# Performance work log

Hardware: AMD Instinct MI355X
Metric: run time of the kernel (lower is better)

The kernel has to match this reference:

```python
import jax, jax.numpy as jnp
import numpy as np

BLANK = 0          # tf.nn.ctc_loss default blank_index (StringLookup reserves 0 for OOV)
PAD = 127          # padding_value = char_to_num.vocabulary_size()
NEG = -1e30        # log-space 'zero' (avoid -inf to keep grads NaN-free)
B, T, C, L = 1024, 256, 128, 32


def setup_inputs() -> dict:
    key = jax.random.key(0)
    k1, k2 = jax.random.split(key)
    # labels in [1, PAD-1]; none equal PAD so label_length == L (full-length labels)
    y_true = jax.random.randint(k1, (B, L), 1, PAD).astype(jnp.int32)
    y_pred = jax.random.normal(k2, (B, T, C), dtype=jnp.float32)
    return {"y_true": y_true, "y_pred": y_pred}


def _ctc_loss(y_true, y_pred):
    """Faithful jax version of tf.nn.ctc_loss(labels, logits, label_len, T,
    logits_time_major=False, blank_index=0): standard log-space alpha DP."""
    Bn, Tn, Cn = y_pred.shape
    Ln = y_true.shape[1]
    S = 2 * Ln + 1  # extended label length (blanks interleaved)

    logp = jax.nn.log_softmax(y_pred, axis=-1)                    # [B,T,C]

    # extended label sequence: blank, l1, blank, l2, ..., blank   # [B,S]
    ext = jnp.full((Bn, S), BLANK, dtype=y_true.dtype)
    ext = ext.at[:, 1::2].set(y_true)

    # log-probs gathered at extended-label symbols                # [B,T,S]
    lp_ext = jnp.take_along_axis(
        logp, jnp.broadcast_to(ext[:, None, :], (Bn, Tn, S)), axis=2)

    # label_length = count of non-padding entries (mirrors count_nonzero)
    label_len = jnp.sum(y_true != PAD, axis=1)                    # [B]

    # skip transition s-2 -> s allowed iff ext[s] is a non-blank differing
    # from ext[s-2]
    skip_ok = jnp.concatenate(
        [jnp.zeros((Bn, 2), bool),
         (ext[:, 2:] != BLANK) & (ext[:, 2:] != ext[:, :-2])], axis=1)  # [B,S]

    neg1 = jnp.full((Bn, 1), NEG, logp.dtype)
    neg2 = jnp.full((Bn, 2), NEG, logp.dtype)

    alpha0 = jnp.full((Bn, S), NEG, logp.dtype)
    alpha0 = alpha0.at[:, 0].set(lp_ext[:, 0, 0]).at[:, 1].set(lp_ext[:, 0, 1])

    def step(alpha, lp_t):  # alpha,[B,S]  lp_t,[B,S]
        a1 = jnp.concatenate([neg1, alpha[:, :-1]], axis=1)
        a2 = jnp.concatenate([neg2, alpha[:, :-2]], axis=1)
        a2 = jnp.where(skip_ok, a2, NEG)
        new = lp_t + jnp.logaddexp(jnp.logaddexp(alpha, a1), a2)
        return new, None

    lp_seq = jnp.transpose(lp_ext, (1, 0, 2))                     # [T,B,S]
    alphaT, _ = jax.lax.scan(step, alpha0, lp_seq[1:])            # [B,S]

    # total log-likelihood ends at last blank (2*len) or last label (2*len-1)
    bi = jnp.arange(Bn)
    e1 = 2 * label_len
    e2 = 2 * label_len - 1
    loglik = jnp.logaddexp(alphaT[bi, e1], alphaT[bi, e2])        # [B]
    return -loglik


def reference(y_true, y_pred):
    # The original layer returns y_pred and registers the loss via add_loss;
    # the compute-dominant quantity is the per-example CTC loss, returned here.
    return _ctc_loss(y_true, y_pred)
```

## Files before the change

### kernel.cpp

```cpp
#include <hip/hip_runtime.h>
#include <cstdint>


#define CTC_BLANK 0
#define CTC_PAD   127
#define NEG       (-1e30f)
#define LOG2E     1.44269504088896340736f
#define LN2       0.69314718055994530942f

constexpr int Bn = 1024, Tn = 256, Cn = 128, Ln = 32;
constexpr int NSLOT = Ln + 1;
constexpr int CR  = 16;
constexpr int NCH = Tn / CR;
constexpr int CF  = CR * Cn;

__device__ __forceinline__ float fexp2(float x) { return __builtin_amdgcn_exp2f(x); }
__device__ __forceinline__ float flog2(float x) { return __builtin_amdgcn_logf(x); }

template <int CTRL>
__device__ __forceinline__ float dpp_add(float s) {
    int v = __builtin_amdgcn_update_dpp(0, __float_as_int(s), CTRL, 0xF, 0xF, true);
    return s + __int_as_float(v);
}
__device__ __forceinline__ float dpp_wave_shr1(float src, float old) {
    return __int_as_float(__builtin_amdgcn_update_dpp(
        __float_as_int(old), __float_as_int(src), 0x138, 0xF, 0xF, false));
}
__device__ __forceinline__ void gl_lds16(const float* g, float* l) {
    __builtin_amdgcn_global_load_lds(
        (const __attribute__((address_space(1))) uint32_t*)g,
        (__attribute__((address_space(3))) uint32_t*)l, 16, 0, 0);
}

__global__ __launch_bounds__(512, 8) void ctc_fused_kernel(
        const int*   __restrict__ y_true,
        const float* __restrict__ y_pred,
        float*       __restrict__ out)
{
    __shared__ __align__(16) float raw[2][CF];
    __shared__ _Float16 Gc[Tn * NSLOT];
    __shared__ int   labels[Ln];
    __shared__ __align__(16) int cmap[Cn];
    __shared__ int   used[Cn];
    __shared__ int   wcnt[8];
    __shared__ float partS[16];

    const int b    = blockIdx.x;
    const int tid  = threadIdx.x;
    const int lane = tid & 63;
    const int wave = tid >> 6;

    const float* gbase = y_pred + (size_t)b * Tn * Cn;

    auto stage = [&](int c, int buf) {
        gl_lds16(gbase + c * CF + tid * 4, &raw[buf][wave * 256]);
    };

    stage(0, 0);

    if (tid < Ln) labels[tid] = y_true[b * Ln + tid];
    if (tid < Cn) used[tid] = 0;
    __syncthreads();
    if (tid == 0) used[CTC_BLANK] = 1;
    if (tid < Ln) used[labels[tid]] = 1;
    __syncthreads();
    {
        bool f = (tid < Cn) && (used[tid] != 0);
        unsigned long long m = __ballot(f);
        if (lane == 0) wcnt[wave] = __popcll(m);
        __syncthreads();
        int base = 0;
        for (int w = 0; w < wave; ++w) base += wcnt[w];
        if (tid < Cn)
            cmap[tid] = f ? (base + __popcll(m & ((1ull << lane) - 1ull))) : -1;
        __syncthreads();
    }

    const int half = lane >> 5;
    const int l32  = lane & 31;
    const int4 cm  = ((const int4*)cmap)[l32];
    float acc = 0.f;

    const int  i      = lane;
    const bool validO = (i < Ln);
    const bool validE = (i <= Ln);
    const int  myLab   = validO ? labels[i] : -1;
    const int  prevLab = (i >= 1 && i < Ln) ? labels[i - 1] : -1;
    const int  slotO   = validO ? cmap[myLab] : 0;
    const bool skipO   = (i >= 1 && i < Ln) &&
                         (myLab != CTC_BLANK) && (myLab != prevLab);
    const int  len = __popcll(__ballot(validO && (myLab != CTC_PAD)));
    float aE = NEG, aO = NEG;

    auto dp_chunk = [&](int t0, int t1) {
        int t = t0;
        if (t == 0) {
            aE = (i == 0) ? (float)Gc[0]     : NEG;
            aO = (i == 0) ? (float)Gc[slotO] : NEG;
            t = 1;
        }
        float pB[2], pO[2];
        const int ta = t, tb = (t + 1 < t1) ? t + 1 : t1 - 1;
        pB[0] = (float)Gc[ta * NSLOT]; pO[0] = (float)Gc[ta * NSLOT + slotO];
        pB[1] = (float)Gc[tb * NSLOT]; pO[1] = (float)Gc[tb * NSLOT + slotO];
        int k = 0;
        #pragma unroll 2
        for (; t < t1; ++t) {
            const float lpB = pB[k], lpO = pO[k];
            const int tp = (t + 2 < t1) ? t + 2 : t1 - 1;
            pB[k] = (float)Gc[tp * NSLOT];
            pO[k] = (float)Gc[tp * NSLOT + slotO];
            k ^= 1;

            const float aOup = dpp_wave_shr1(aO, NEG);
            const float m  = fmaxf(aE, aOup);
            const float e1 = fexp2(aE - m);
            const float e2 = fexp2(aOup - m);
            const float sE = e1 + e2;
            const float nE = lpB + m + flog2(sE);
            const float m3 = fmaxf(aO, m);
            const float nO = lpO + m3 +
                flog2(fexp2(aO - m3) + (skipO ? sE : e1) * fexp2(m - m3));
            aE = validE ? nE : NEG;
            aO = validO ? nO : NEG;
        }
    };

    for (int c = 0; c < NCH; ++c) {
        if (c + 1 < NCH) stage(c + 1, (c + 1) & 1);

        if (wave == 0 && c > 0) dp_chunk((c - 1) * CR, c * CR);

        __builtin_amdgcn_sched_barrier(0);
        if (c + 1 < NCH) asm volatile("s_waitcnt vmcnt(1)" ::: "memory");
        else             asm volatile("s_waitcnt vmcnt(0)" ::: "memory");
        __builtin_amdgcn_sched_barrier(0);

        {
            const int rl = 2 * wave + half;
            const int r  = c * CR + rl;
            const float4 x = ((const float4*)&raw[c & 1][rl * Cn])[l32];
            const float e0 = x.x * LOG2E, e1 = x.y * LOG2E,
                        e2 = x.z * LOG2E, e3 = x.w * LOG2E;
            if (cm.x >= 0) Gc[r * NSLOT + cm.x] = (_Float16)e0;
            if (cm.y >= 0) Gc[r * NSLOT + cm.y] = (_Float16)e1;
            if (cm.z >= 0) Gc[r * NSLOT + cm.z] = (_Float16)e2;
            if (cm.w >= 0) Gc[r * NSLOT + cm.w] = (_Float16)e3;
            float s = fexp2(e0) + fexp2(e1) + fexp2(e2) + fexp2(e3);
            s = dpp_add<0x111>(s);
            s = dpp_add<0x112>(s);
            s = dpp_add<0x114>(s);
            s = dpp_add<0x118>(s);
            s = dpp_add<0x142>(s);
            acc += flog2(s);
        }
        if (c == NCH - 1 && l32 == 31) partS[wave * 2 + half] = acc;

        asm volatile("s_waitcnt lgkmcnt(0)" ::: "memory");
        __builtin_amdgcn_s_barrier();
    }

    if (wave == 0) {
        dp_chunk(Tn - CR, Tn);
        const float v1 = __shfl(aE, len, 64);
        const float v2 = __shfl(aO, len - 1, 64);
        if (i == 0) {
            float S = 0.f;
            #pragma unroll
            for (int j = 0; j < 16; ++j) S += partS[j];
            const float mm = fmaxf(v1, v2);
            const float L2 = mm + flog2(fexp2(v1 - mm) + fexp2(v2 - mm));
            out[b] = LN2 * (S - L2);
        }
    }
}

extern "C" void kernel_launch(void* const* d_in, const int* in_sizes, int n_in,
                              void* d_out, int out_size, void* d_ws, size_t ws_size,
                              hipStream_t stream) {
    const int*   y_true = (const int*)d_in[0];
    const float* y_pred = (const float*)d_in[1];
    float*       out    = (float*)d_out;
    ctc_fused_kernel<<<Bn, 512, 0, stream>>>(y_true, y_pred, out);
}
```

Before: 202.1 us.

## Deepen per-wave prefetch to four stages and batch DP into four phases

Each wave now owns a private ring of four LDS staging slots and keeps several global-to-LDS loads in flight. This removes the block-wide barrier that previously sat between every 16-row chunk. The alpha DP in wave 0 now runs only at four phase boundaries over 64 timesteps each, so only four block barriers remain. The aim is more memory-level parallelism and less synchronisation, at the cost of more LDS per block (the occupancy hint drops from 8 to 6) and longer serial DP stretches while the other waves idle.

New measurement: 214.1 us. +5.9%, slower.

```diff
diff --git a/kernel.cpp b/kernel.cpp
--- a/kernel.cpp
+++ b/kernel.cpp
@@ -10,9 +10,12 @@
 
 constexpr int Bn = 1024, Tn = 256, Cn = 128, Ln = 32;
 constexpr int NSLOT = Ln + 1;
-constexpr int CR  = 16;
-constexpr int NCH = Tn / CR;
-constexpr int CF  = CR * Cn;
+constexpr int CR    = 16;
+constexpr int NIT   = Tn / CR;
+constexpr int DEPTH = 4;
+constexpr int PH    = 4;
+constexpr int IPP   = NIT / PH;
+constexpr int TPP   = Tn / PH;
 
 __device__ __forceinline__ float fexp2(float x) { return __builtin_amdgcn_exp2f(x); }
 __device__ __forceinline__ float flog2(float x) { return __builtin_amdgcn_logf(x); }
@@ -32,12 +35,12 @@
         (__attribute__((address_space(3))) uint32_t*)l, 16, 0, 0);
 }
 
-__global__ __launch_bounds__(512, 8) void ctc_fused_kernel(
+__global__ __launch_bounds__(512, 6) void ctc_fused_kernel(
         const int*   __restrict__ y_true,
         const float* __restrict__ y_pred,
         float*       __restrict__ out)
 {
-    __shared__ __align__(16) float raw[2][CF];
+    __shared__ __align__(16) float raw[8][DEPTH][256];
     __shared__ _Float16 Gc[Tn * NSLOT];
     __shared__ int   labels[Ln];
     __shared__ __align__(16) int cmap[Cn];
@@ -52,11 +55,13 @@
 
     const float* gbase = y_pred + (size_t)b * Tn * Cn;
 
-    auto stage = [&](int c, int buf) {
-        gl_lds16(gbase + c * CF + tid * 4, &raw[buf][wave * 256]);
+    auto stage = [&](int j) {
+        gl_lds16(gbase + (size_t)(j * CR + 2 * wave) * Cn + lane * 4,
+                 &raw[wave][j & (DEPTH - 1)][0]);
     };
 
-    stage(0, 0);
+    #pragma unroll
+    for (int j0 = 0; j0 < DEPTH; ++j0) stage(j0);
 
     if (tid < Ln) labels[tid] = y_true[b * Ln + tid];
     if (tid < Cn) used[tid] = 0;
@@ -126,20 +131,19 @@
         }
     };
 
-    for (int c = 0; c < NCH; ++c) {
-        if (c + 1 < NCH) stage(c + 1, (c + 1) & 1);
+    for (int p = 0; p < PH; ++p) {
+        for (int q = 0; q < IPP; ++q) {
+            const int j   = p * IPP + q;
+            const int rem = (NIT - 1) - j;
+            if (rem >= DEPTH - 1) asm volatile("s_waitcnt vmcnt(3)" ::: "memory");
+            else if (rem == 2)    asm volatile("s_waitcnt vmcnt(2)" ::: "memory");
+            else if (rem == 1)    asm volatile("s_waitcnt vmcnt(1)" ::: "memory");
+            else                  asm volatile("s_waitcnt vmcnt(0)" ::: "memory");
 
-        if (wave == 0 && c > 0) dp_chunk((c - 1) * CR, c * CR);
-
-        __builtin_amdgcn_sched_barrier(0);
-        if (c + 1 < NCH) asm volatile("s_waitcnt vmcnt(1)" ::: "memory");
-        else             asm volatile("s_waitcnt vmcnt(0)" ::: "memory");
-        __builtin_amdgcn_sched_barrier(0);
-
-        {
-            const int rl = 2 * wave + half;
-            const int r  = c * CR + rl;
-            const float4 x = ((const float4*)&raw[c & 1][rl * Cn])[l32];
+            const int slot = j & (DEPTH - 1);
+            const int r    = j * CR + 2 * wave + half;
+            const float4 x =
+                ((const float4*)&raw[wave][slot][0])[half * 32 + l32];
             const float e0 = x.x * LOG2E, e1 = x.y * LOG2E,
                         e2 = x.z * LOG2E, e3 = x.w * LOG2E;
             if (cm.x >= 0) Gc[r * NSLOT + cm.x] = (_Float16)e0;
@@ -153,15 +157,20 @@
             s = dpp_add<0x118>(s);
             s = dpp_add<0x142>(s);
             acc += flog2(s);
+            if (j == NIT - 1 && l32 == 31) partS[wave * 2 + half] = acc;
+
+            asm volatile("s_waitcnt lgkmcnt(0)" ::: "memory");
+            if (j + DEPTH < NIT) stage(j + DEPTH);
         }
-        if (c == NCH - 1 && l32 == 31) partS[wave * 2 + half] = acc;
+
+        if (wave == 0 && p > 0) dp_chunk((p - 1) * TPP, p * TPP);
 
         asm volatile("s_waitcnt lgkmcnt(0)" ::: "memory");
         __builtin_amdgcn_s_barrier();
     }
 
     if (wave == 0) {
-        dp_chunk(Tn - CR, Tn);
+        dp_chunk(Tn - TPP, Tn);
         const float v1 = __shfl(aE, len, 64);
         const float v2 = __shfl(aO, len - 1, 64);
         if (i == 0) {
```

## Split CTC into softmax kernel and packed 4-waves-per-block DP kernel via workspace

Applied to the files above, without the earlier changes.

Replaces the single fused kernel, in which one wave per block ran the serial alpha recursion while the others streamed logits, with two kernels. The first computes the log-sum-exp and writes the gathered log-probs as a slot-major fp16 table to the workspace. The second runs the DP with four batch items per 256-thread block and vectorised h4 loads. This is meant to stop the serial DP from holding a 512-thread block resident, and to let many more DP waves run concurrently. In exchange it adds a global round trip for the gathered table (about 17 MB), a second launch, and a dependence on the workspace size, with the old fused kernel kept as a fallback.

Result: slower. 227.3 us (+12.5%).

```diff
diff --git a/kernel.cpp b/kernel.cpp
--- a/kernel.cpp
+++ b/kernel.cpp
@@ -10,9 +10,13 @@
 
 constexpr int Bn = 1024, Tn = 256, Cn = 128, Ln = 32;
 constexpr int NSLOT = Ln + 1;
-constexpr int CR  = 16;
-constexpr int NCH = Tn / CR;
-constexpr int CF  = CR * Cn;
+constexpr int GSLOT = 34;
+constexpr int GT_B  = GSLOT * Tn;
+
+constexpr size_t WS_GT   = 0;
+constexpr size_t WS_SLOT = (size_t)Bn * GT_B * 2;
+constexpr size_t WS_S    = WS_SLOT + (size_t)Bn * Ln * 4;
+constexpr size_t WS_NEED = WS_S + (size_t)Bn * 4;
 
 __device__ __forceinline__ float fexp2(float x) { return __builtin_amdgcn_exp2f(x); }
 __device__ __forceinline__ float flog2(float x) { return __builtin_amdgcn_logf(x); }
@@ -32,7 +36,180 @@
         (__attribute__((address_space(3))) uint32_t*)l, 16, 0, 0);
 }
 
-__global__ __launch_bounds__(512, 8) void ctc_fused_kernel(
+__global__ __launch_bounds__(512, 8) void ctc_softmax_kernel(
+        const int*   __restrict__ y_true,
+        const float* __restrict__ y_pred,
+        _Float16*    __restrict__ Gt,
+        int*         __restrict__ slotO_arr,
+        float*       __restrict__ Sglob)
+{
+    __shared__ int labels[Ln];
+    __shared__ __align__(16) int cmap[Cn];
+    __shared__ int used[Cn];
+    __shared__ int wcnt[8];
+    __shared__ float partS[16];
+
+    const int b    = blockIdx.x;
+    const int tid  = threadIdx.x;
+    const int lane = tid & 63;
+    const int wave = tid >> 6;
+    const int half = lane >> 5;
+    const int l32  = lane & 31;
+
+    const float4* gsrc = (const float4*)(y_pred + (size_t)b * Tn * Cn);
+    float4 xr0 = gsrc[tid];
+    float4 xr1 = gsrc[512  + tid];
+    float4 xr2 = gsrc[1024 + tid];
+    float4 xr3 = gsrc[1536 + tid];
+
+    if (tid < Ln) labels[tid] = y_true[b * Ln + tid];
+    if (tid < Cn) used[tid] = 0;
+    __syncthreads();
+    if (tid == 0) used[CTC_BLANK] = 1;
+    if (tid < Ln) used[labels[tid]] = 1;
+    __syncthreads();
+    {
+        bool f = (tid < Cn) && (used[tid] != 0);
+        unsigned long long m = __ballot(f);
+        if (lane == 0) wcnt[wave] = __popcll(m);
+        __syncthreads();
+        int base = 0;
+        for (int w = 0; w < wave; ++w) base += wcnt[w];
+        if (tid < Cn)
+            cmap[tid] = f ? (base + __popcll(m & ((1ull << lane) - 1ull))) : -1;
+        __syncthreads();
+    }
+
+    const int4 cm = ((const int4*)cmap)[l32];
+    _Float16* gt = Gt + (size_t)b * GT_B;
+    const int rbase = tid >> 5;
+    float acc = 0.f;
+
+    #pragma unroll
+    for (int j = 0; j < 16; ++j) {
+        float4 x;
+        if      ((j & 3) == 0) x = xr0;
+        else if ((j & 3) == 1) x = xr1;
+        else if ((j & 3) == 2) x = xr2;
+        else                   x = xr3;
+        if (j + 4 < 16) {
+            float4 nx = gsrc[(j + 4) * 512 + tid];
+            if      ((j & 3) == 0) xr0 = nx;
+            else if ((j & 3) == 1) xr1 = nx;
+            else if ((j & 3) == 2) xr2 = nx;
+            else                   xr3 = nx;
+        }
+        const float e0 = x.x * LOG2E, e1 = x.y * LOG2E,
+                    e2 = x.z * LOG2E, e3 = x.w * LOG2E;
+        const int tcol = j * 16 + rbase;
+        if (cm.x >= 0) gt[cm.x * Tn + tcol] = (_Float16)e0;
+        if (cm.y >= 0) gt[cm.y * Tn + tcol] = (_Float16)e1;
+        if (cm.z >= 0) gt[cm.z * Tn + tcol] = (_Float16)e2;
+        if (cm.w >= 0) gt[cm.w * Tn + tcol] = (_Float16)e3;
+        float s = fexp2(e0) + fexp2(e1) + fexp2(e2) + fexp2(e3);
+        s = dpp_add<0x111>(s);
+        s = dpp_add<0x112>(s);
+        s = dpp_add<0x114>(s);
+        s = dpp_add<0x118>(s);
+        s = dpp_add<0x142>(s);
+        acc += flog2(s);
+    }
+    if (l32 == 31) partS[wave * 2 + half] = acc;
+    if (tid < Ln) slotO_arr[b * Ln + tid] = cmap[labels[tid]];
+    __syncthreads();
+    if (tid == 0) {
+        float S = 0.f;
+        #pragma unroll
+        for (int j = 0; j < 16; ++j) S += partS[j];
+        Sglob[b] = S;
+    }
+}
+
+typedef __attribute__((ext_vector_type(4))) _Float16 h4;
+
+__global__ __launch_bounds__(256) void ctc_dp_kernel(
+        const int*      __restrict__ y_true,
+        const _Float16* __restrict__ Gt,
+        const int*      __restrict__ slotO_arr,
+        const float*    __restrict__ Sglob,
+        float*          __restrict__ out)
+{
+    const int wave = threadIdx.x >> 6;
+    const int i    = threadIdx.x & 63;
+    const int b    = blockIdx.x * 4 + wave;
+    if (b >= Bn) return;
+
+    const bool validO = (i < Ln);
+    const bool validE = (i <= Ln);
+    const int  myLab   = validO ? y_true[b * Ln + i] : -1;
+    const int  prevLab = (i >= 1 && i < Ln) ? y_true[b * Ln + i - 1] : -1;
+    const int  slotO   = validO ? slotO_arr[b * Ln + i] : 0;
+    const bool skipO   = (i >= 1 && i < Ln) &&
+                         (myLab != CTC_BLANK) && (myLab != prevLab);
+    const int  len = __popcll(__ballot(validO && (myLab != CTC_PAD)));
+
+    const _Float16* gB = Gt + (size_t)b * GT_B;
+    const _Float16* gO = gB + slotO * Tn;
+
+    float aE = (i == 0) ? (float)gB[0] : NEG;
+    float aO = (i == 0) ? (float)gO[0] : NEG;
+
+    auto step = [&](float lpB, float lpO) {
+        const float aOup = dpp_wave_shr1(aO, NEG);
+        const float m  = fmaxf(aE, aOup);
+        const float e1 = fexp2(aE - m);
+        const float e2 = fexp2(aOup - m);
+        const float sE = e1 + e2;
+        const float nE = lpB + m + flog2(sE);
+        const float m3 = fmaxf(aO, m);
+        const float nO = lpO + m3 +
+            flog2(fexp2(aO - m3) + (skipO ? sE : e1) * fexp2(m - m3));
+        aE = validE ? nE : NEG;
+        aO = validO ? nO : NEG;
+    };
+
+    h4 vB0 = *(const h4*)(gB),     vB1 = *(const h4*)(gB + 4);
+    h4 vO0 = *(const h4*)(gO),     vO1 = *(const h4*)(gO + 4);
+    {
+        h4 nB0 = *(const h4*)(gB + 8),  nB1 = *(const h4*)(gB + 12);
+        h4 nO0 = *(const h4*)(gO + 8),  nO1 = *(const h4*)(gO + 12);
+        #pragma unroll
+        for (int k = 1; k < 4; ++k) step((float)vB0[k], (float)vO0[k]);
+        #pragma unroll
+        for (int k = 0; k < 4; ++k) step((float)vB1[k], (float)vO1[k]);
+        vB0 = nB0; vB1 = nB1; vO0 = nO0; vO1 = nO1;
+    }
+    for (int g = 1; g < 31; ++g) {
+        h4 nB0 = *(const h4*)(gB + 8 * (g + 1));
+        h4 nB1 = *(const h4*)(gB + 8 * (g + 1) + 4);
+        h4 nO0 = *(const h4*)(gO + 8 * (g + 1));
+        h4 nO1 = *(const h4*)(gO + 8 * (g + 1) + 4);
+        #pragma unroll
+        for (int k = 0; k < 4; ++k) step((float)vB0[k], (float)vO0[k]);
+        #pragma unroll
+        for (int k = 0; k < 4; ++k) step((float)vB1[k], (float)vO1[k]);
+        vB0 = nB0; vB1 = nB1; vO0 = nO0; vO1 = nO1;
+    }
+    #pragma unroll
+    for (int k = 0; k < 4; ++k) step((float)vB0[k], (float)vO0[k]);
+    #pragma unroll
+    for (int k = 0; k < 4; ++k) step((float)vB1[k], (float)vO1[k]);
+
+    const float v1 = __shfl(aE, len, 64);
+    const float v2 = __shfl(aO, len - 1, 64);
+    if (i == 0) {
+        const float S  = Sglob[b];
+        const float mm = fmaxf(v1, v2);
+        const float L2 = mm + flog2(fexp2(v1 - mm) + fexp2(v2 - mm));
+        out[b] = LN2 * (S - L2);
+    }
+}
+
+constexpr int CR  = 16;
+constexpr int NCH = Tn / CR;
+constexpr int CF  = CR * Cn;
+
+__global__ __launch_bounds__(512, 8) void ctc_fused_fallback(
         const int*   __restrict__ y_true,
         const float* __restrict__ y_pred,
         float*       __restrict__ out)
@@ -51,11 +228,9 @@
     const int wave = tid >> 6;
 
     const float* gbase = y_pred + (size_t)b * Tn * Cn;
-
     auto stage = [&](int c, int buf) {
         gl_lds16(gbase + c * CF + tid * 4, &raw[buf][wave * 256]);
     };
-
     stage(0, 0);
 
     if (tid < Ln) labels[tid] = y_true[b * Ln + tid];
@@ -111,7 +286,6 @@
             pB[k] = (float)Gc[tp * NSLOT];
             pO[k] = (float)Gc[tp * NSLOT + slotO];
             k ^= 1;
-
             const float aOup = dpp_wave_shr1(aO, NEG);
             const float m  = fmaxf(aE, aOup);
             const float e1 = fexp2(aE - m);
@@ -128,14 +302,11 @@
 
     for (int c = 0; c < NCH; ++c) {
         if (c + 1 < NCH) stage(c + 1, (c + 1) & 1);
-
         if (wave == 0 && c > 0) dp_chunk((c - 1) * CR, c * CR);
-
         __builtin_amdgcn_sched_barrier(0);
         if (c + 1 < NCH) asm volatile("s_waitcnt vmcnt(1)" ::: "memory");
         else             asm volatile("s_waitcnt vmcnt(0)" ::: "memory");
         __builtin_amdgcn_sched_barrier(0);
-
         {
             const int rl = 2 * wave + half;
             const int r  = c * CR + rl;
@@ -155,7 +326,6 @@
             acc += flog2(s);
         }
         if (c == NCH - 1 && l32 == 31) partS[wave * 2 + half] = acc;
-
         asm volatile("s_waitcnt lgkmcnt(0)" ::: "memory");
         __builtin_amdgcn_s_barrier();
     }
@@ -181,5 +351,13 @@
     const int*   y_true = (const int*)d_in[0];
     const float* y_pred = (const float*)d_in[1];
     float*       out    = (float*)d_out;
-    ctc_fused_kernel<<<Bn, 512, 0, stream>>>(y_true, y_pred, out);
-}
+    if (d_ws != nullptr && ws_size >= WS_NEED) {
+        _Float16* Gt    = (_Float16*)((char*)d_ws + WS_GT);
+        int*      slotO = (int*)((char*)d_ws + WS_SLOT);
+        float*    Sg    = (float*)((char*)d_ws + WS_S);
+        ctc_softmax_kernel<<<Bn, 512, 0, stream>>>(y_true, y_pred, Gt, slotO, Sg);
+        ctc_dp_kernel<<<Bn / 4, 256, 0, stream>>>(y_true, Gt, slotO, Sg, out);
+    } else {
+        ctc_fused_fallback<<<Bn, 512, 0, stream>>>(y_true, y_pred, out);
+    }
+}
```
